# Kernel tuning notes

Measured on AMD Instinct MI355X. Metric: run time of the kernel, lower is better.

## Reference

```python
import jax, jax.numpy as jnp
import numpy as np
from jax import lax

EPS = 1e-5
K = 3  # DCN kernel size


def _conv(x, w, pad, lhs_dil=(1, 1)):
    return lax.conv_general_dilated(
        x, w, window_strides=(1, 1), padding=((pad, pad), (pad, pad)),
        lhs_dilation=lhs_dil, dimension_numbers=('NCHW', 'OIHW', 'NCHW'))


def _batchnorm(x, gamma, beta):
    # training-mode BN (batch statistics), matching nn.BatchNorm2d in train()
    m = jnp.mean(x, axis=(0, 2, 3), keepdims=True)
    v = jnp.var(x, axis=(0, 2, 3), keepdims=True)
    return (x - m) * lax.rsqrt(v + EPS) * gamma[None, :, None, None] + beta[None, :, None, None]


def _bilinear_sample(x, py, px):
    # x: [B,C,H,W]; py,px: [B,K2,H,W] fractional sample coords (zero-pad outside)
    B, C, H, W = x.shape
    K2 = py.shape[1]
    y0 = jnp.floor(py)
    x0 = jnp.floor(px)
    wy = (py - y0)[:, None]  # [B,1,K2,H,W]
    wx = (px - x0)[:, None]
    xf = x.reshape(B, C, H * W)

    def gather(yi, xi):
        valid = ((yi >= 0) & (yi <= H - 1) & (xi >= 0) & (xi <= W - 1)).astype(x.dtype)
        yc = jnp.clip(yi, 0, H - 1).astype(jnp.int32)
        xc = jnp.clip(xi, 0, W - 1).astype(jnp.int32)
        idx = (yc * W + xc).reshape(B, 1, -1)
        v = jnp.take_along_axis(xf, idx, axis=2).reshape(B, C, K2, H, W)
        return v * valid[:, None]

    v00 = gather(y0, x0)
    v01 = gather(y0, x0 + 1)
    v10 = gather(y0 + 1, x0)
    v11 = gather(y0 + 1, x0 + 1)
    return (v00 * (1 - wy) * (1 - wx) + v01 * (1 - wy) * wx
            + v10 * wy * (1 - wx) + v11 * wy * wx)  # [B,C,K2,H,W]


def _dcn(x, w_off, b_off, w_dcn, b_dcn):
    # Modulated deformable conv (DCNv2), stride 1, pad 1, dil 1, 1 deform group
    B, C, H, W = x.shape
    K2 = K * K
    om = _conv(x, w_off, pad=1) + b_off[None, :, None, None]  # [B,3*K2,H,W]
    dy, dx, m = om[:, :K2], om[:, K2:2 * K2], jax.nn.sigmoid(om[:, 2 * K2:])
    ki, kj = jnp.meshgrid(jnp.arange(K), jnp.arange(K), indexing='ij')
    ky = (ki.reshape(-1) - 1).astype(x.dtype)[None, :, None, None]
    kx = (kj.reshape(-1) - 1).astype(x.dtype)[None, :, None, None]
    py = dy + jnp.arange(H, dtype=x.dtype)[None, None, :, None] + ky
    px = dx + jnp.arange(W, dtype=x.dtype)[None, None, None, :] + kx
    val = _bilinear_sample(x, py, px) * m[:, None]  # [B,C,K2,H,W]
    Co = w_dcn.shape[0]
    out = jnp.einsum('bikhw,oik->bohw', val, w_dcn.reshape(Co, C, K2))
    return out + b_dcn[None, :, None, None]


def _conv_transpose(x, w_up):
    # torch ConvTranspose2d(k=4, stride=2, pad=1), weight [Cin, Cout, 4, 4]
    w = jnp.flip(w_up, axis=(2, 3)).transpose(1, 0, 2, 3)  # -> OIHW
    return _conv(x, w, pad=2, lhs_dil=(2, 2))


def setup_inputs() -> dict:
    key = jax.random.key(0)
    ks = jax.random.split(key, 8)
    B, Cin, Cout, H, W = 4, 256, 256, 64, 64
    x = jax.random.normal(ks[0], (B, Cin, H, W), dtype=jnp.float32)
    w_off = jax.random.normal(ks[1], (3 * K * K, Cin, K, K), dtype=jnp.float32) * 0.01
    b_off = jnp.zeros((3 * K * K,), dtype=jnp.float32)
    w_dcn = jax.random.normal(ks[2], (Cout, Cin, K, K), dtype=jnp.float32) * (1.0 / np.sqrt(Cin * K * K))
    b_dcn = jnp.zeros((Cout,), dtype=jnp.float32)
    gamma1 = jax.random.uniform(ks[3], (Cout,), dtype=jnp.float32, minval=0.5, maxval=1.5)
    beta1 = jax.random.normal(ks[4], (Cout,), dtype=jnp.float32) * 0.1
    w_up = jax.random.normal(ks[5], (Cout, Cout, 4, 4), dtype=jnp.float32) * (1.0 / np.sqrt(Cout * 16))
    gamma2 = jax.random.uniform(ks[6], (Cout,), dtype=jnp.float32, minval=0.5, maxval=1.5)
    beta2 = jax.random.normal(ks[7], (Cout,), dtype=jnp.float32) * 0.1
    return {'x': x, 'w_off': w_off, 'b_off': b_off, 'w_dcn': w_dcn, 'b_dcn': b_dcn,
            'gamma1': gamma1, 'beta1': beta1, 'w_up': w_up, 'gamma2': gamma2, 'beta2': beta2}


def reference(x, w_off, b_off, w_dcn, b_dcn, gamma1, beta1, w_up, gamma2, beta2):
    out = _dcn(x, w_off, b_off, w_dcn, b_dcn)
    out = jax.nn.relu(_batchnorm(out, gamma1, beta1))
    out = _conv_transpose(out, w_up)
    out = jax.nn.relu(_batchnorm(out, gamma2, beta2))
    return out
```

## Files before the change

### kernel.cpp

```cpp
#include <hip/hip_runtime.h>
#include <hip/hip_bf16.h>
#include <math.h>

#define B_   4
#define CIN  256
#define COUT 256
#define HW   4096

typedef __attribute__((ext_vector_type(8))) short short8;
typedef __attribute__((ext_vector_type(4))) float float4v;

#define LSTR  40
#define LSTR2 72
#define LSTR4 136

__device__ __forceinline__ float sigmoidf_(float v){ return 1.0f/(1.0f+expf(-v)); }
__device__ __forceinline__ ushort f2bf(float f){
  union { float f; unsigned u; } x; x.f = f;
  unsigned r = x.u + 0x7fffu + ((x.u>>16)&1u);
  return (ushort)(r>>16);
}
__device__ __forceinline__ float bflo(unsigned u){ union{unsigned u; float f;} c; c.u = u<<16;          return c.f; }
__device__ __forceinline__ float bfhi(unsigned u){ union{unsigned u; float f;} c; c.u = u & 0xffff0000u; return c.f; }

__global__ void k_transpose_x(const float* __restrict__ x, ushort* __restrict__ xtb){
  __shared__ float ts[32][33];
  int tx = threadIdx.x & 31, ty = threadIdx.x >> 5;
  int p0 = blockIdx.x * 32, c0 = blockIdx.y * 32, b = blockIdx.z;
  const float* xb = x + (size_t)b*CIN*HW;
#pragma unroll
  for(int q=0;q<4;q++){
    int c = ty + q*8;
    ts[c][tx] = xb[(size_t)(c0+c)*HW + p0+tx];
  }
  __syncthreads();
#pragma unroll
  for(int q=0;q<4;q++){
    int pr = ty + q*8;
    xtb[((size_t)(b*HW + p0+pr)<<8) + c0+tx] = f2bf(ts[tx][pr]);
  }
}

__global__ void k_build_all(const float* __restrict__ w_off, const float* __restrict__ w_dcn,
                            const float* __restrict__ w_up,
                            ushort* __restrict__ Wob, ushort* __restrict__ Wdb,
                            ushort* __restrict__ WT2c){
  int bid = blockIdx.x;
  if(bid < 288){
    int f = bid*256 + threadIdx.x;
    int kc = f>>10, o = (f>>5)&31, kk = f&31;
    int k = kc*32 + kk, tap = k>>8, c = k&255;
    float v = (o < 27) ? w_off[(size_t)o*2304 + c*9 + tap] : 0.f;
    Wob[f] = f2bf(v);
  } else if(bid < 288+2304){
    int f = (bid-288)*256 + threadIdx.x;
    int kc = f>>13, o = (f>>5)&255, kk = f&31;
    int k = kc>>3, c = ((kc&7)<<5) | kk;
    Wdb[f] = f2bf(w_dcn[(size_t)o*2304 + c*9 + k]);
  } else {
    int f = (bid-2592)*256 + threadIdx.x;
    int pp = f>>18, kc = (f>>13)&31, o = (f>>5)&255, kk = f&31;
    int k = kc*32 + kk, ab = k>>8, c = k&255;
    int a = ab>>1, bb = ab&1, ph = pp>>1, pw = pp&1;
    WT2c[f] = f2bf(w_up[(size_t)(c*COUT+o)*16 + (3-ph-2*a)*4 + (3-pw-2*bb)]);
  }
}

__global__ __launch_bounds__(256) void k_offset_mfma(const ushort* __restrict__ xtb,
                        const ushort* __restrict__ Wob, float* __restrict__ om2){
  __shared__ ushort Vs[2][64*LSTR4];
  __shared__ int sIdx[576];
  int tid = threadIdx.x;
  int fb  = blockIdx.x + (blockIdx.y<<6);
  int b   = (fb&7)>>1;
  int px0 = ((((fb>>3)<<1) | (fb&1))) << 6;
  int z   = blockIdx.z;
  for(int t=tid; t<576; t+=256){
    int tap = t>>6, px = t&63;
    int p = px0+px, hh = p>>6, ww = p&63;
    int ih = hh + tap/3 - 1, iw = ww + tap%3 - 1;
    sIdx[t] = (ih>=0 && ih<64 && iw>=0 && iw<64) ? ((b*HW + ih*64+iw)<<8) : -1;
  }
  __syncthreads();

  int lane = tid&63, wv = tid>>6, lo = lane&15, hi = lane>>4;
  float4v acc[2];
  acc[0] = acc[1] = (float4v){0.f,0.f,0.f,0.f};
  int vpx = tid>>2, vseg = tid&3;
  const int wlane = lo*32 + hi*8;

#define OFF_WLOAD_ALLQ(Q, W) do{ \
    _Pragma("unroll") \
    for(int c_=0;c_<4;c_++){ \
      const ushort* wp_ = Wob + (((Q)*4+c_)<<10) + wlane; \
      W[2*c_+0] = *(const short8*)(wp_); \
      W[2*c_+1] = *(const short8*)(wp_ + 512); \
    } \
  }while(0)

#define OFF_GATHER_Q(Q, V) do{ \
    int k_ = (Q)>>1, c0_ = ((Q)&1)<<7; \
    int idx_ = sIdx[(k_<<6)+vpx]; \
    int coff_ = c0_ + (vseg<<5); \
    V[0]=make_uint4(0,0,0,0); V[1]=make_uint4(0,0,0,0); \
    V[2]=make_uint4(0,0,0,0); V[3]=make_uint4(0,0,0,0); \
    if(idx_ >= 0){ \
      V[0] = *(const uint4*)(xtb + idx_ + coff_); \
      V[1] = *(const uint4*)(xtb + idx_ + coff_ + 8); \
      V[2] = *(const uint4*)(xtb + idx_ + coff_ + 16); \
      V[3] = *(const uint4*)(xtb + idx_ + coff_ + 24); \
    } \
  }while(0)

#define OFF_VWRITE_Q(V, BUF) do{ \
    ushort* vp_ = &Vs[BUF][vpx*LSTR4 + (vseg<<5)]; \
    *(uint4*)(vp_)      = V[0]; \
    *(uint4*)(vp_ + 8)  = V[1]; \
    *(uint4*)(vp_ + 16) = V[2]; \
    *(uint4*)(vp_ + 24) = V[3]; \
  }while(0)

#define OFF_COMPUTE_Q2(W, BUF) do{ \
    const ushort* bp_ = &Vs[BUF][(wv*16+lo)*LSTR4 + hi*8]; \
    _Pragma("unroll") \
    for(int c_=0;c_<4;c_++){ \
      short8 ba_ = *(const short8*)(bp_ + c_*32); \
      acc[0] = __builtin_amdgcn_mfma_f32_16x16x32_bf16(W[2*c_+0], ba_, acc[0], 0,0,0); \
      acc[1] = __builtin_amdgcn_mfma_f32_16x16x32_bf16(W[2*c_+1], ba_, acc[1], 0,0,0); \
    } \
  }while(0)

  short8 w[8];
  uint4 vE[4];
  OFF_GATHER_Q(z*9, vE);
  OFF_VWRITE_Q(vE, 0);
  __syncthreads();

#pragma unroll 1
  for(int pc=0; pc<9; ++pc){
    int cur = pc&1;
    int q = z*9 + pc;
    OFF_WLOAD_ALLQ(q, w);
    if(pc<8) OFF_GATHER_Q(q+1, vE);
    OFF_COMPUTE_Q2(w, cur);
    if(pc<8) OFF_VWRITE_Q(vE, cur^1);
    __syncthreads();
  }
  int p = px0 + wv*16 + lo;
#pragma unroll
  for(int mi=0;mi<2;mi++){
    int ob = mi*16 + hi*4;
    float4v a = (mi==0) ? acc[0] : acc[1];
#pragma unroll
    for(int r=0;r<4;r++){
      int o = ob + r;
      if(o < 27) om2[(size_t)((z*B_+b)*27+o)*HW + p] = a[r];
    }
  }
}

#define DCN_WLOAD_ALLQ(Q, W) do{ \
    _Pragma("unroll") \
    for(int c_=0;c_<4;c_++){ \
      const ushort* wp_ = Wdb + ((size_t)((Q)*4+c_)<<13) + wlane; \
      W[4*c_+0] = *(const short8*)(wp_); \
      W[4*c_+1] = *(const short8*)(wp_ + 512); \
      W[4*c_+2] = *(const short8*)(wp_ + 1024); \
      W[4*c_+3] = *(const short8*)(wp_ + 1536); \
    } \
  }while(0)

#define DCN_GATHER_Q(Q, C, CF) do{ \
    int k_ = (Q)>>1, c0_ = ((Q)&1)<<7; \
    int t_ = (k_<<6) + vpx; \
    int pk_ = sPk[t_]; CF = sCf[t_]; \
    int coff_ = c0_ + (vseg<<4); \
    int iy0_=pk_&63, iy1_=(pk_>>6)&63, ix0_=(pk_>>12)&63, ix1_=(pk_>>18)&63; \
    const ushort* p00_ = xtb + cbase + (((iy0_<<6)+ix0_)<<8) + coff_; \
    const ushort* p01_ = xtb + cbase + (((iy0_<<6)+ix1_)<<8) + coff_; \
    const ushort* p10_ = xtb + cbase + (((iy1_<<6)+ix0_)<<8) + coff_; \
    const ushort* p11_ = xtb + cbase + (((iy1_<<6)+ix1_)<<8) + coff_; \
    C[0] = *(const uint4*)(p00_);     C[4] = *(const uint4*)(p00_ + 8); \
    C[1] = *(const uint4*)(p01_);     C[5] = *(const uint4*)(p01_ + 8); \
    C[2] = *(const uint4*)(p10_);     C[6] = *(const uint4*)(p10_ + 8); \
    C[3] = *(const uint4*)(p11_);     C[7] = *(const uint4*)(p11_ + 8); \
  }while(0)

#define DCN_BLEND_H(C0,C1,C2,C3, CF, DST) do{ \
    union{ ushort us[8]; uint4 q; } rr_; \
    rr_.us[0] = f2bf(CF.x*bflo(C0.x)+CF.y*bflo(C1.x)+CF.z*bflo(C2.x)+CF.w*bflo(C3.x)); \
    rr_.us[1] = f2bf(CF.x*bfhi(C0.x)+CF.y*bfhi(C1.x)+CF.z*bfhi(C2.x)+CF.w*bfhi(C3.x)); \
    rr_.us[2] = f2bf(CF.x*bflo(C0.y)+CF.y*bflo(C1.y)+CF.z*bflo(C2.y)+CF.w*bflo(C3.y)); \
    rr_.us[3] = f2bf(CF.x*bfhi(C0.y)+CF.y*bfhi(C1.y)+CF.z*bfhi(C2.y)+CF.w*bfhi(C3.y)); \
    rr_.us[4] = f2bf(CF.x*bflo(C0.z)+CF.y*bflo(C1.z)+CF.z*bflo(C2.z)+CF.w*bflo(C3.z)); \
    rr_.us[5] = f2bf(CF.x*bfhi(C0.z)+CF.y*bfhi(C1.z)+CF.z*bfhi(C2.z)+CF.w*bfhi(C3.z)); \
    rr_.us[6] = f2bf(CF.x*bflo(C0.w)+CF.y*bflo(C1.w)+CF.z*bflo(C2.w)+CF.w*bflo(C3.w)); \
    rr_.us[7] = f2bf(CF.x*bfhi(C0.w)+CF.y*bfhi(C1.w)+CF.z*bfhi(C2.w)+CF.w*bfhi(C3.w)); \
    *(uint4*)(DST) = rr_.q; \
  }while(0)

#define DCN_BLEND_Q(C, CF, BUF) do{ \
    ushort* dp_ = &Vs[BUF][vpx*LSTR4 + (vseg<<4)]; \
    DCN_BLEND_H(C[0],C[1],C[2],C[3], CF, dp_); \
    DCN_BLEND_H(C[4],C[5],C[6],C[7], CF, dp_ + 8); \
  }while(0)

#define DCN_COMPUTE_Q2(W, BUF) do{ \
    const ushort* bp_ = &Vs[BUF][(pn0+lo)*LSTR4 + hi*8]; \
    _Pragma("unroll") \
    for(int c_=0;c_<4;c_++){ \
      short8 b0_ = *(const short8*)(bp_ + c_*32); \
      short8 b1_ = *(const short8*)(bp_ + c_*32 + 16*LSTR4); \
      acc[0][0] = __builtin_amdgcn_mfma_f32_16x16x32_bf16(W[4*c_+0], b0_, acc[0][0], 0,0,0); \
      acc[0][1] = __builtin_amdgcn_mfma_f32_16x16x32_bf16(W[4*c_+0], b1_, acc[0][1], 0,0,0); \
      acc[1][0] = __builtin_amdgcn_mfma_f32_16x16x32_bf16(W[4*c_+1], b0_, acc[1][0], 0,0,0); \
      acc[1][1] = __builtin_amdgcn_mfma_f32_16x16x32_bf16(W[4*c_+1], b1_, acc[1][1], 0,0,0); \
      acc[2][0] = __builtin_amdgcn_mfma_f32_16x16x32_bf16(W[4*c_+2], b0_, acc[2][0], 0,0,0); \
      acc[2][1] = __builtin_amdgcn_mfma_f32_16x16x32_bf16(W[4*c_+2], b1_, acc[2][1], 0,0,0); \
      acc[3][0] = __builtin_amdgcn_mfma_f32_16x16x32_bf16(W[4*c_+3], b0_, acc[3][0], 0,0,0); \
      acc[3][1] = __builtin_amdgcn_mfma_f32_16x16x32_bf16(W[4*c_+3], b1_, acc[3][1], 0,0,0); \
    } \
  }while(0)

__global__ __launch_bounds__(512) void k_dcn_mfma(const ushort* __restrict__ xtb,
                        const float* __restrict__ om2, const float* __restrict__ b_off,
                        const ushort* __restrict__ Wdb, ushort* __restrict__ out1u){
  __shared__ ushort Vs[2][64*LSTR4];
  __shared__ int    sPk[576];
  __shared__ float4 sCf[576];
  int tid = threadIdx.x;
  int fb  = blockIdx.x + (blockIdx.y<<6);
  int b   = (fb&7)>>1;
  int px0 = ((((fb>>3)<<1) | (fb&1))) << 6;
  int z   = blockIdx.z;

  for(int t=tid; t<576; t+=512){
    int k = t>>6, px = t&63;
    int p = px0 + px, hh = p>>6, ww = p&63;
    const float* oma = om2 + (size_t)b*27*HW + p;
    const float* omb = oma + (size_t)B_*27*HW;
    float dy = oma[(size_t)k*HW]      + omb[(size_t)k*HW]      + b_off[k];
    float dx = oma[(size_t)(9+k)*HW]  + omb[(size_t)(9+k)*HW]  + b_off[9+k];
    float mo = sigmoidf_(oma[(size_t)(18+k)*HW] + omb[(size_t)(18+k)*HW] + b_off[18+k]);
    float py  = dy + (float)(hh + k/3 - 1);
    float pxf = dx + (float)(ww + k%3 - 1);
    float y0 = floorf(py), x0 = floorf(pxf);
    float wy = py - y0, wx = pxf - x0;
    float y1 = y0 + 1.0f, x1 = x0 + 1.0f;
    bool vy0 = (y0>=0.f)&&(y0<=63.f), vy1 = (y1>=0.f)&&(y1<=63.f);
    bool vx0 = (x0>=0.f)&&(x0<=63.f), vx1 = (x1>=0.f)&&(x1<=63.f);
    int iy0 = (int)fminf(fmaxf(y0,0.f),63.f);
    int iy1 = (int)fminf(fmaxf(y1,0.f),63.f);
    int ix0 = (int)fminf(fmaxf(x0,0.f),63.f);
    int ix1 = (int)fminf(fmaxf(x1,0.f),63.f);
    sPk[t] = iy0 | (iy1<<6) | (ix0<<12) | (ix1<<18);
    sCf[t] = make_float4((vy0&&vx0)? (1.f-wy)*(1.f-wx)*mo : 0.f,
                         (vy0&&vx1)? (1.f-wy)*wx*mo       : 0.f,
                         (vy1&&vx0)? wy*(1.f-wx)*mo       : 0.f,
                         (vy1&&vx1)? wy*wx*mo             : 0.f);
  }
  __syncthreads();

  int lane = tid&63, wv = tid>>6, lo = lane&15, hi = lane>>4;
  int om0 = (wv>>1)*64, pn0 = (wv&1)*32;
  float4v acc[4][2];
#pragma unroll
  for(int i=0;i<4;i++)
#pragma unroll
    for(int j=0;j<2;j++) acc[i][j] = (float4v){0.f,0.f,0.f,0.f};
  int cbase = (b*HW)<<8;
  int vpx = tid>>3, vseg = tid&7;
  const int wlane = (om0+lo)*32 + hi*8;

  short8 w[16];
  uint4 cE[8];
  float4 fE;

  DCN_GATHER_Q(z*9, cE, fE);
  DCN_BLEND_Q(cE, fE, 0);
  __syncthreads();

#pragma unroll 1
  for(int pc=0; pc<9; ++pc){
    int cur = pc&1;
    int q = z*9 + pc;
    DCN_WLOAD_ALLQ(q, w);
    if(pc<8) DCN_GATHER_Q(q+1, cE, fE);
    DCN_COMPUTE_Q2(w, cur);
    if(pc<8) DCN_BLEND_Q(cE, fE, cur^1);
    __syncthreads();
  }

  ushort* op0 = out1u + ((size_t)((z*B_+b)*COUT)<<12) + px0 + pn0 + lo;
#pragma unroll
  for(int i=0;i<4;i++){
    int ob = om0 + i*16 + hi*4;
#pragma unroll
    for(int r=0;r<4;r++){
      int o = ob + r;
      ushort* op = op0 + ((size_t)o<<12);
#pragma unroll
      for(int j=0;j<2;j++) op[j*16] = f2bf(acc[i][j][r]);
    }
  }
}

__global__ void k_bn_stats_bf2(const ushort* __restrict__ out1u, float* __restrict__ stats){
  int o = blockIdx.x, tid = threadIdx.x;
  float s=0.f, ss=0.f;
  for(int b=0;b<B_;b++){
    const ushort* pa = out1u + ((size_t)(b*COUT+o)<<12);
    const ushort* pb = pa + ((size_t)B_*COUT<<12);
    for(int i=tid*8; i<4096; i+=2048){
      uint4 va = *(const uint4*)(pa + i);
      uint4 vb = *(const uint4*)(pb + i);
      float f;
      f=bflo(va.x)+bflo(vb.x); s+=f; ss+=f*f;  f=bfhi(va.x)+bfhi(vb.x); s+=f; ss+=f*f;
      f=bflo(va.y)+bflo(vb.y); s+=f; ss+=f*f;  f=bfhi(va.y)+bfhi(vb.y); s+=f; ss+=f*f;
      f=bflo(va.z)+bflo(vb.z); s+=f; ss+=f*f;  f=bfhi(va.z)+bfhi(vb.z); s+=f; ss+=f*f;
      f=bflo(va.w)+bflo(vb.w); s+=f; ss+=f*f;  f=bfhi(va.w)+bfhi(vb.w); s+=f; ss+=f*f;
    }
  }
  __shared__ float rs[256], rss[256];
  rs[tid]=s; rss[tid]=ss; __syncthreads();
  for(int st=128; st>0; st>>=1){
    if(tid<st){ rs[tid]+=rs[tid+st]; rss[tid]+=rss[tid+st]; }
    __syncthreads();
  }
  if(tid==0){
    float n = (float)(B_*HW);
    float mean = rs[0]/n;
    float var  = rss[0]/n - mean*mean;
    stats[o*2] = mean; stats[o*2+1] = rsqrtf(var + 1e-5f);
  }
}

__global__ void k_bn_stats_ct(const ushort* __restrict__ ct, float* __restrict__ stats){
  int o = blockIdx.x, tid = threadIdx.x;
  float s=0.f, ss=0.f;
  for(int pl=0; pl<16; ++pl){
    const ushort* p = ct + (((size_t)(pl*256 + o))<<12);
    for(int i=tid*8; i<4096; i+=2048){
      uint4 v = *(const uint4*)(p + i);
      float f;
      f=bflo(v.x); s+=f; ss+=f*f;  f=bfhi(v.x); s+=f; ss+=f*f;
      f=bflo(v.y); s+=f; ss+=f*f;  f=bfhi(v.y); s+=f; ss+=f*f;
      f=bflo(v.z); s+=f; ss+=f*f;  f=bfhi(v.z); s+=f; ss+=f*f;
      f=bflo(v.w); s+=f; ss+=f*f;  f=bfhi(v.w); s+=f; ss+=f*f;
    }
  }
  __shared__ float rs[256], rss[256];
  rs[tid]=s; rss[tid]=ss; __syncthreads();
  for(int st=128; st>0; st>>=1){
    if(tid<st){ rs[tid]+=rs[tid+st]; rss[tid]+=rss[tid+st]; }
    __syncthreads();
  }
  if(tid==0){
    float n = (float)(16*4096);
    float mean = rs[0]/n;
    float var  = rss[0]/n - mean*mean;
    stats[o*2] = mean; stats[o*2+1] = rsqrtf(var + 1e-5f);
  }
}

__global__ void k_bn1_apply_t(const ushort* __restrict__ out1u, const float* __restrict__ stats,
                              const float* __restrict__ gamma, const float* __restrict__ beta,
                              ushort* __restrict__ y1b){
  __shared__ float ts[32][33];
  int tx = threadIdx.x & 31, ty = threadIdx.x >> 5;
  int p0 = blockIdx.x*32, o0 = blockIdx.y*32, b = blockIdx.z;
#pragma unroll
  for(int q=0;q<4;q++){
    int oo = ty + q*8; int o = o0 + oo;
    float m = stats[o*2], rstd = stats[o*2+1];
    float scale = rstd * gamma[o];
    float shift = beta[o] - m * scale;
    size_t idx = ((size_t)(b*COUT+o)<<12) + p0+tx;
    float v = bflo((unsigned)out1u[idx]) + bflo((unsigned)out1u[idx + ((size_t)B_*COUT<<12)]);
    ts[oo][tx] = fmaxf(v*scale + shift, 0.f);
  }
  __syncthreads();
#pragma unroll
  for(int q=0;q<4;q++){
    int pr = ty + q*8;
    y1b[((size_t)(b*HW + p0+pr)<<8) + o0+tx] = f2bf(ts[tx][pr]);
  }
}

__global__ __launch_bounds__(512) void k_convt_mfma(const ushort* __restrict__ y1b,
                        const ushort* __restrict__ WT2c,
                        ushort* __restrict__ ct){
  __shared__ ushort Vs[2][256*LSTR2];
  __shared__ int sIdx[1024];
  int tid = threadIdx.x;
  int fb  = blockIdx.x + (blockIdx.y<<4) + (blockIdx.z<<6);
  int jj = fb&7, rr2 = fb>>3;
  int b   = jj>>1;
  int pp  = ((rr2>>4)<<1) | (jj&1);
  int px0 = (rr2&15) << 8;
  int ph = pp>>1, pw = pp&1;

  for(int t=tid; t<1024; t+=512){
    int ab = t>>8, px = t&255;
    int a = ab>>1, bb = ab&1;
    int p = px0+px, r = p>>6, s = p&63;
    int ih = r + ph - 1 + a, iw = s + pw - 1 + bb;
    sIdx[t] = (ih>=0 && ih<64 && iw>=0 && iw<64) ? ((b*HW + ih*64+iw)<<8) : -1;
  }
  __syncthreads();

  int lane = tid&63, wv = tid>>6, lo = lane&15, hi = lane>>4;
  int om0 = (wv>>1)*64;
  int pn0 = (wv&1)*128;
  float4v acc[4][8];
#pragma unroll
  for(int i=0;i<4;i++)
#pragma unroll
    for(int j=0;j<8;j++) acc[i][j] = (float4v){0.f,0.f,0.f,0.f};

  const ushort* wbase = WT2c + ((size_t)pp<<18);
  const int wlaneb = (om0+lo)*32 + hi*8;
  int vpx = tid>>1, vseg = tid&1;
  uint4 vpre[4];

#define CT3_PREFETCH(PC) do{ \
    int kc0_ = (PC)*2; \
    int ab_ = kc0_>>3, c0_ = (kc0_&7)<<5; \
    int idx_ = sIdx[(ab_<<8) + vpx]; \
    int co_ = c0_ + vseg*32; \
    vpre[0]=make_uint4(0,0,0,0); vpre[1]=make_uint4(0,0,0,0); \
    vpre[2]=make_uint4(0,0,0,0); vpre[3]=make_uint4(0,0,0,0); \
    if(idx_ >= 0){ \
      vpre[0] = *(const uint4*)(y1b + idx_ + co_); \
      vpre[1] = *(const uint4*)(y1b + idx_ + co_ + 8); \
      vpre[2] = *(const uint4*)(y1b + idx_ + co_ + 16); \
      vpre[3] = *(const uint4*)(y1b + idx_ + co_ + 24); \
    } \
  }while(0)

#define CT3_WRITE(BUF) do{ \
    ushort* vp_ = &Vs[BUF][vpx*LSTR2 + vseg*32]; \
    *(uint4*)(vp_)      = vpre[0]; \
    *(uint4*)(vp_ + 8)  = vpre[1]; \
    *(uint4*)(vp_ + 16) = vpre[2]; \
    *(uint4*)(vp_ + 24) = vpre[3]; \
  }while(0)

  CT3_PREFETCH(0);
  CT3_WRITE(0);
  __syncthreads();

#pragma unroll 1
  for(int pc=0; pc<16; ++pc){
    int cur = pc&1;
    if(pc < 15) CT3_PREFETCH(pc+1);
#pragma unroll
    for(int c=0; c<2; ++c){
      const ushort* wp = wbase + ((size_t)(((pc<<1)|c))<<13) + wlaneb;
      const ushort* bp = &Vs[cur][(pn0+lo)*LSTR2 + c*32 + hi*8];
      short8 bfr[8];
#pragma unroll
      for(int j=0;j<8;j++) bfr[j] = *(const short8*)(bp + j*16*LSTR2);
#pragma unroll
      for(int i=0;i<4;i++){
        short8 afr = *(const short8*)(wp + i*512);
#pragma unroll
        for(int j=0;j<8;j++)
          acc[i][j] = __builtin_amdgcn_mfma_f32_16x16x32_bf16(afr, bfr[j], acc[i][j], 0,0,0);
      }
    }
    if(pc < 15) CT3_WRITE(cur^1);
    __syncthreads();
  }

  ushort* cb = ct + (((size_t)(pp*4 + b)*256)<<12);
#pragma unroll
  for(int i=0;i<4;i++){
#pragma unroll
    for(int r=0;r<4;r++){
      int o = om0 + i*16 + hi*4 + r;
      ushort* row = cb + ((size_t)o<<12) + px0 + pn0 + lo;
#pragma unroll
      for(int j=0;j<8;j++) row[j*16] = f2bf(acc[i][j][r]);
    }
  }
}

__global__ void k_bn2_apply(const ushort* __restrict__ ct, const float* __restrict__ stats,
                            const float* __restrict__ gamma, const float* __restrict__ beta,
                            float* __restrict__ out){
  int gid = blockIdx.x*256 + threadIdx.x;
  int e4 = gid<<2;
  int b = e4>>22, o = (e4>>14)&255, q = e4&16383;
  int H2 = q>>7, W2 = q&127;
  int r = H2>>1, ph = H2&1, s0 = W2>>1;
  size_t base0 = (((size_t)((ph*2)*4 + b)*256 + o)<<12) + r*64 + s0;
  unsigned u0 = *(const unsigned*)(ct + base0);
  unsigned u1 = *(const unsigned*)(ct + base0 + ((size_t)4<<20));
  float m = stats[o*2], rstd = stats[o*2+1];
  float sc = rstd * gamma[o];
  float sh = beta[o] - m * sc;
  float4 v;
  v.x = fmaxf(bflo(u0)*sc + sh, 0.f);
  v.y = fmaxf(bflo(u1)*sc + sh, 0.f);
  v.z = fmaxf(bfhi(u0)*sc + sh, 0.f);
  v.w = fmaxf(bfhi(u1)*sc + sh, 0.f);
  *(float4*)(out + e4) = v;
}

extern "C" void kernel_launch(void* const* d_in, const int* in_sizes, int n_in,
                              void* d_out, int out_size, void* d_ws, size_t ws_size,
                              hipStream_t stream){
  (void)in_sizes; (void)n_in; (void)out_size; (void)ws_size;
  const float* x     = (const float*)d_in[0];
  const float* w_off = (const float*)d_in[1];
  const float* b_off = (const float*)d_in[2];
  const float* w_dcn = (const float*)d_in[3];
  const float* gamma1= (const float*)d_in[5];
  const float* beta1 = (const float*)d_in[6];
  const float* w_up  = (const float*)d_in[7];
  const float* gamma2= (const float*)d_in[8];
  const float* beta2 = (const float*)d_in[9];
  float* out = (float*)d_out;

  float* ws    = (float*)d_ws;
  ushort* ct   = (ushort*)ws;
  float* om2   = ws;
  ushort* xtb  = (ushort*)(ws + 884736);
  ushort* out1u= (ushort*)(ws + 884736 + 2097152);
  float* base2 = ws + 8388608;
  ushort* y1b  = (ushort*)base2;
  ushort* WT2c = (ushort*)(base2 + 2097152);
  ushort* Wdb  = (ushort*)(base2 + 2097152 + 524288);
  ushort* Wob  = (ushort*)(base2 + 2097152 + 524288 + 294912);
  float* st1   = base2 + 2097152 + 524288 + 294912 + 36864;
  float* st2   = st1 + 512;

  k_transpose_x <<<dim3(128,8,4), 256, 0, stream>>>(x, xtb);
  k_build_all   <<<6688, 256, 0, stream>>>(w_off, w_dcn, w_up, Wob, Wdb, WT2c);
  k_offset_mfma <<<dim3(64,4,2), 256, 0, stream>>>(xtb, Wob, om2);
  k_dcn_mfma    <<<dim3(64,4,2), 512, 0, stream>>>(xtb, om2, b_off, Wdb, out1u);
  k_bn_stats_bf2<<<256,  256, 0, stream>>>(out1u, st1);
  k_bn1_apply_t <<<dim3(128,8,4), 256, 0, stream>>>(out1u, st1, gamma1, beta1, y1b);
  k_convt_mfma  <<<dim3(16,4,4),  512, 0, stream>>>(y1b, WT2c, ct);
  k_bn_stats_ct <<<256,  256, 0, stream>>>(ct, st2);
  k_bn2_apply   <<<16384,256, 0, stream>>>(ct, st2, gamma2, beta2, out);
}
```

Measured before the change: 257.6 us.

## Fuse BN statistics into GEMM epilogues and drop DCN split-K

Batch-norm sum and sum-of-squares are now accumulated with wave shuffles and atomics in the epilogues of the DCN and transposed-conv kernels, so the two separate stats kernels and their re-reads of the outputs go away. The DCN kernel no longer splits K across two z-slices; each block runs all 18 chunks and writes a single output, so bn1_apply reads only one buffer. The trade-off is half as many DCN blocks (less parallelism), float atomic contention, and variance computed from raw sums in fp32.

```diff
diff --git a/kernel.cpp b/kernel.cpp
--- a/kernel.cpp
+++ b/kernel.cpp
@@ -44,8 +44,14 @@
 __global__ void k_build_all(const float* __restrict__ w_off, const float* __restrict__ w_dcn,
                             const float* __restrict__ w_up,
                             ushort* __restrict__ Wob, ushort* __restrict__ Wdb,
-                            ushort* __restrict__ WT2c){
+                            ushort* __restrict__ WT2c,
+                            float* __restrict__ st1raw, float* __restrict__ st2raw){
   int bid = blockIdx.x;
+  if(bid == 0 && threadIdx.x < 256){
+    int t = threadIdx.x;
+    st1raw[t] = 0.f; st1raw[256+t] = 0.f;
+    st2raw[t] = 0.f; st2raw[256+t] = 0.f;
+  }
   if(bid < 288){
     int f = bid*256 + threadIdx.x;
     int kc = f>>10, o = (f>>5)&31, kk = f&31;
@@ -224,7 +230,8 @@
 
 __global__ __launch_bounds__(512) void k_dcn_mfma(const ushort* __restrict__ xtb,
                         const float* __restrict__ om2, const float* __restrict__ b_off,
-                        const ushort* __restrict__ Wdb, ushort* __restrict__ out1u){
+                        const ushort* __restrict__ Wdb, ushort* __restrict__ out1u,
+                        float* __restrict__ st1raw){
   __shared__ ushort Vs[2][64*LSTR4];
   __shared__ int    sPk[576];
   __shared__ float4 sCf[576];
@@ -232,7 +239,6 @@
   int fb  = blockIdx.x + (blockIdx.y<<6);
   int b   = (fb&7)>>1;
   int px0 = ((((fb>>3)<<1) | (fb&1))) << 6;
-  int z   = blockIdx.z;
 
   for(int t=tid; t<576; t+=512){
     int k = t>>6, px = t&63;
@@ -276,22 +282,21 @@
   uint4 cE[8];
   float4 fE;
 
-  DCN_GATHER_Q(z*9, cE, fE);
+  DCN_GATHER_Q(0, cE, fE);
   DCN_BLEND_Q(cE, fE, 0);
   __syncthreads();
 
 #pragma unroll 1
-  for(int pc=0; pc<9; ++pc){
+  for(int pc=0; pc<18; ++pc){
     int cur = pc&1;
-    int q = z*9 + pc;
-    DCN_WLOAD_ALLQ(q, w);
-    if(pc<8) DCN_GATHER_Q(q+1, cE, fE);
+    DCN_WLOAD_ALLQ(pc, w);
+    if(pc<17) DCN_GATHER_Q(pc+1, cE, fE);
     DCN_COMPUTE_Q2(w, cur);
-    if(pc<8) DCN_BLEND_Q(cE, fE, cur^1);
+    if(pc<17) DCN_BLEND_Q(cE, fE, cur^1);
     __syncthreads();
   }
 
-  ushort* op0 = out1u + ((size_t)((z*B_+b)*COUT)<<12) + px0 + pn0 + lo;
+  ushort* op0 = out1u + ((size_t)(b*COUT)<<12) + px0 + pn0 + lo;
 #pragma unroll
   for(int i=0;i<4;i++){
     int ob = om0 + i*16 + hi*4;
@@ -299,84 +304,37 @@
     for(int r=0;r<4;r++){
       int o = ob + r;
       ushort* op = op0 + ((size_t)o<<12);
-#pragma unroll
-      for(int j=0;j<2;j++) op[j*16] = f2bf(acc[i][j][r]);
+      float v0 = acc[i][0][r], v1 = acc[i][1][r];
+      op[0]  = f2bf(v0);
+      op[16] = f2bf(v1);
+      float s  = v0 + v1;
+      float q2 = v0*v0 + v1*v1;
+#pragma unroll
+      for(int st=1; st<16; st<<=1){ s += __shfl_xor(s, st); q2 += __shfl_xor(q2, st); }
+      if(lo == 0){
+        atomicAdd(&st1raw[2*o],   s);
+        atomicAdd(&st1raw[2*o+1], q2);
+      }
     }
   }
 }
 
-__global__ void k_bn_stats_bf2(const ushort* __restrict__ out1u, float* __restrict__ stats){
-  int o = blockIdx.x, tid = threadIdx.x;
-  float s=0.f, ss=0.f;
-  for(int b=0;b<B_;b++){
-    const ushort* pa = out1u + ((size_t)(b*COUT+o)<<12);
-    const ushort* pb = pa + ((size_t)B_*COUT<<12);
-    for(int i=tid*8; i<4096; i+=2048){
-      uint4 va = *(const uint4*)(pa + i);
-      uint4 vb = *(const uint4*)(pb + i);
-      float f;
-      f=bflo(va.x)+bflo(vb.x); s+=f; ss+=f*f;  f=bfhi(va.x)+bfhi(vb.x); s+=f; ss+=f*f;
-      f=bflo(va.y)+bflo(vb.y); s+=f; ss+=f*f;  f=bfhi(va.y)+bfhi(vb.y); s+=f; ss+=f*f;
-      f=bflo(va.z)+bflo(vb.z); s+=f; ss+=f*f;  f=bfhi(va.z)+bfhi(vb.z); s+=f; ss+=f*f;
-      f=bflo(va.w)+bflo(vb.w); s+=f; ss+=f*f;  f=bfhi(va.w)+bfhi(vb.w); s+=f; ss+=f*f;
-    }
-  }
-  __shared__ float rs[256], rss[256];
-  rs[tid]=s; rss[tid]=ss; __syncthreads();
-  for(int st=128; st>0; st>>=1){
-    if(tid<st){ rs[tid]+=rs[tid+st]; rss[tid]+=rss[tid+st]; }
-    __syncthreads();
-  }
-  if(tid==0){
-    float n = (float)(B_*HW);
-    float mean = rs[0]/n;
-    float var  = rss[0]/n - mean*mean;
-    stats[o*2] = mean; stats[o*2+1] = rsqrtf(var + 1e-5f);
-  }
-}
-
-__global__ void k_bn_stats_ct(const ushort* __restrict__ ct, float* __restrict__ stats){
-  int o = blockIdx.x, tid = threadIdx.x;
-  float s=0.f, ss=0.f;
-  for(int pl=0; pl<16; ++pl){
-    const ushort* p = ct + (((size_t)(pl*256 + o))<<12);
-    for(int i=tid*8; i<4096; i+=2048){
-      uint4 v = *(const uint4*)(p + i);
-      float f;
-      f=bflo(v.x); s+=f; ss+=f*f;  f=bfhi(v.x); s+=f; ss+=f*f;
-      f=bflo(v.y); s+=f; ss+=f*f;  f=bfhi(v.y); s+=f; ss+=f*f;
-      f=bflo(v.z); s+=f; ss+=f*f;  f=bfhi(v.z); s+=f; ss+=f*f;
-      f=bflo(v.w); s+=f; ss+=f*f;  f=bfhi(v.w); s+=f; ss+=f*f;
-    }
-  }
-  __shared__ float rs[256], rss[256];
-  rs[tid]=s; rss[tid]=ss; __syncthreads();
-  for(int st=128; st>0; st>>=1){
-    if(tid<st){ rs[tid]+=rs[tid+st]; rss[tid]+=rss[tid+st]; }
-    __syncthreads();
-  }
-  if(tid==0){
-    float n = (float)(16*4096);
-    float mean = rs[0]/n;
-    float var  = rss[0]/n - mean*mean;
-    stats[o*2] = mean; stats[o*2+1] = rsqrtf(var + 1e-5f);
-  }
-}
-
-__global__ void k_bn1_apply_t(const ushort* __restrict__ out1u, const float* __restrict__ stats,
+__global__ void k_bn1_apply_t(const ushort* __restrict__ out1u, const float* __restrict__ st1raw,
                               const float* __restrict__ gamma, const float* __restrict__ beta,
                               ushort* __restrict__ y1b){
   __shared__ float ts[32][33];
   int tx = threadIdx.x & 31, ty = threadIdx.x >> 5;
   int p0 = blockIdx.x*32, o0 = blockIdx.y*32, b = blockIdx.z;
+  const float inv_n = 1.f/16384.f;
 #pragma unroll
   for(int q=0;q<4;q++){
     int oo = ty + q*8; int o = o0 + oo;
-    float m = stats[o*2], rstd = stats[o*2+1];
+    float mean = st1raw[2*o] * inv_n;
+    float var  = st1raw[2*o+1] * inv_n - mean*mean;
+    float rstd = rsqrtf(var + 1e-5f);
     float scale = rstd * gamma[o];
-    float shift = beta[o] - m * scale;
-    size_t idx = ((size_t)(b*COUT+o)<<12) + p0+tx;
-    float v = bflo((unsigned)out1u[idx]) + bflo((unsigned)out1u[idx + ((size_t)B_*COUT<<12)]);
+    float shift = beta[o] - mean * scale;
+    float v = bflo((unsigned)out1u[((size_t)(b*COUT+o)<<12) + p0+tx]);
     ts[oo][tx] = fmaxf(v*scale + shift, 0.f);
   }
   __syncthreads();
@@ -389,7 +347,7 @@
 
 __global__ __launch_bounds__(512) void k_convt_mfma(const ushort* __restrict__ y1b,
                         const ushort* __restrict__ WT2c,
-                        ushort* __restrict__ ct){
+                        ushort* __restrict__ ct, float* __restrict__ st2raw){
   __shared__ ushort Vs[2][256*LSTR2];
   __shared__ int sIdx[1024];
   int tid = threadIdx.x;
@@ -480,13 +438,24 @@
     for(int r=0;r<4;r++){
       int o = om0 + i*16 + hi*4 + r;
       ushort* row = cb + ((size_t)o<<12) + px0 + pn0 + lo;
-#pragma unroll
-      for(int j=0;j<8;j++) row[j*16] = f2bf(acc[i][j][r]);
+      float s = 0.f, q2 = 0.f;
+#pragma unroll
+      for(int j=0;j<8;j++){
+        float v = acc[i][j][r];
+        row[j*16] = f2bf(v);
+        s += v; q2 += v*v;
+      }
+#pragma unroll
+      for(int st=1; st<16; st<<=1){ s += __shfl_xor(s, st); q2 += __shfl_xor(q2, st); }
+      if(lo == 0){
+        atomicAdd(&st2raw[2*o],   s);
+        atomicAdd(&st2raw[2*o+1], q2);
+      }
     }
   }
 }
 
-__global__ void k_bn2_apply(const ushort* __restrict__ ct, const float* __restrict__ stats,
+__global__ void k_bn2_apply(const ushort* __restrict__ ct, const float* __restrict__ st2raw,
                             const float* __restrict__ gamma, const float* __restrict__ beta,
                             float* __restrict__ out){
   int gid = blockIdx.x*256 + threadIdx.x;
@@ -497,9 +466,11 @@
   size_t base0 = (((size_t)((ph*2)*4 + b)*256 + o)<<12) + r*64 + s0;
   unsigned u0 = *(const unsigned*)(ct + base0);
   unsigned u1 = *(const unsigned*)(ct + base0 + ((size_t)4<<20));
-  float m = stats[o*2], rstd = stats[o*2+1];
+  const float inv_n = 1.f/65536.f;
+  float mean = st2raw[2*o] * inv_n;
+  float rstd = rsqrtf(st2raw[2*o+1]*inv_n - mean*mean + 1e-5f);
   float sc = rstd * gamma[o];
-  float sh = beta[o] - m * sc;
+  float sh = beta[o] - mean * sc;
   float4 v;
   v.x = fmaxf(bflo(u0)*sc + sh, 0.f);
   v.y = fmaxf(bflo(u1)*sc + sh, 0.f);
@@ -533,16 +504,14 @@
   ushort* WT2c = (ushort*)(base2 + 2097152);
   ushort* Wdb  = (ushort*)(base2 + 2097152 + 524288);
   ushort* Wob  = (ushort*)(base2 + 2097152 + 524288 + 294912);
-  float* st1   = base2 + 2097152 + 524288 + 294912 + 36864;
-  float* st2   = st1 + 512;
+  float* st1raw= base2 + 2097152 + 524288 + 294912 + 36864;
+  float* st2raw= st1raw + 512;
 
   k_transpose_x <<<dim3(128,8,4), 256, 0, stream>>>(x, xtb);
-  k_build_all   <<<6688, 256, 0, stream>>>(w_off, w_dcn, w_up, Wob, Wdb, WT2c);
+  k_build_all   <<<6688, 256, 0, stream>>>(w_off, w_dcn, w_up, Wob, Wdb, WT2c, st1raw, st2raw);
   k_offset_mfma <<<dim3(64,4,2), 256, 0, stream>>>(xtb, Wob, om2);
-  k_dcn_mfma    <<<dim3(64,4,2), 512, 0, stream>>>(xtb, om2, b_off, Wdb, out1u);
-  k_bn_stats_bf2<<<256,  256, 0, stream>>>(out1u, st1);
-  k_bn1_apply_t <<<dim3(128,8,4), 256, 0, stream>>>(out1u, st1, gamma1, beta1, y1b);
-  k_convt_mfma  <<<dim3(16,4,4),  512, 0, stream>>>(y1b, WT2c, ct);
-  k_bn_stats_ct <<<256,  256, 0, stream>>>(ct, st2);
-  k_bn2_apply   <<<16384,256, 0, stream>>>(ct, st2, gamma2, beta2, out);
-}
+  k_dcn_mfma    <<<dim3(64,4),   512, 0, stream>>>(xtb, om2, b_off, Wdb, out1u, st1raw);
+  k_bn1_apply_t <<<dim3(128,8,4), 256, 0, stream>>>(out1u, st1raw, gamma1, beta1, y1b);
+  k_convt_mfma  <<<dim3(16,4,4),  512, 0, stream>>>(y1b, WT2c, ct, st2raw);
+  k_bn2_apply   <<<16384,256, 0, stream>>>(ct, st2raw, gamma2, beta2, out);
+}
```

Result: slower. 519.1 us (+101.5%).

## Drop split-K in deformable conv; accumulate all 18 chunks per block

Applied to the files above, without the earlier changes.

The DCN MFMA kernel no longer splits the reduction over two z-slices that wrote separate bf16 partial outputs. Each block now loops over all 18 chunks and writes a single output, so the BN stats and BN apply kernels read one buffer instead of summing two. This removes the extra partial-output write and read traffic and one bf16 rounding step. In exchange the grid is halved to 256 blocks, which reduces parallelism and latency hiding on the GPU.

```diff
diff --git a/kernel.cpp b/kernel.cpp
--- a/kernel.cpp
+++ b/kernel.cpp
@@ -232,7 +232,6 @@
   int fb  = blockIdx.x + (blockIdx.y<<6);
   int b   = (fb&7)>>1;
   int px0 = ((((fb>>3)<<1) | (fb&1))) << 6;
-  int z   = blockIdx.z;
 
   for(int t=tid; t<576; t+=512){
     int k = t>>6, px = t&63;
@@ -276,22 +275,21 @@
   uint4 cE[8];
   float4 fE;
 
-  DCN_GATHER_Q(z*9, cE, fE);
+  DCN_GATHER_Q(0, cE, fE);
   DCN_BLEND_Q(cE, fE, 0);
   __syncthreads();
 
 #pragma unroll 1
-  for(int pc=0; pc<9; ++pc){
+  for(int pc=0; pc<18; ++pc){
     int cur = pc&1;
-    int q = z*9 + pc;
-    DCN_WLOAD_ALLQ(q, w);
-    if(pc<8) DCN_GATHER_Q(q+1, cE, fE);
+    DCN_WLOAD_ALLQ(pc, w);
+    if(pc<17) DCN_GATHER_Q(pc+1, cE, fE);
     DCN_COMPUTE_Q2(w, cur);
-    if(pc<8) DCN_BLEND_Q(cE, fE, cur^1);
+    if(pc<17) DCN_BLEND_Q(cE, fE, cur^1);
     __syncthreads();
   }
 
-  ushort* op0 = out1u + ((size_t)((z*B_+b)*COUT)<<12) + px0 + pn0 + lo;
+  ushort* op0 = out1u + ((size_t)(b*COUT)<<12) + px0 + pn0 + lo;
 #pragma unroll
   for(int i=0;i<4;i++){
     int ob = om0 + i*16 + hi*4;
@@ -299,26 +297,24 @@
     for(int r=0;r<4;r++){
       int o = ob + r;
       ushort* op = op0 + ((size_t)o<<12);
-#pragma unroll
-      for(int j=0;j<2;j++) op[j*16] = f2bf(acc[i][j][r]);
+      op[0]  = f2bf(acc[i][0][r]);
+      op[16] = f2bf(acc[i][1][r]);
     }
   }
 }
 
-__global__ void k_bn_stats_bf2(const ushort* __restrict__ out1u, float* __restrict__ stats){
+__global__ void k_bn_stats_bf1(const ushort* __restrict__ out1u, float* __restrict__ stats){
   int o = blockIdx.x, tid = threadIdx.x;
   float s=0.f, ss=0.f;
   for(int b=0;b<B_;b++){
-    const ushort* pa = out1u + ((size_t)(b*COUT+o)<<12);
-    const ushort* pb = pa + ((size_t)B_*COUT<<12);
+    const ushort* p = out1u + ((size_t)(b*COUT+o)<<12);
     for(int i=tid*8; i<4096; i+=2048){
-      uint4 va = *(const uint4*)(pa + i);
-      uint4 vb = *(const uint4*)(pb + i);
+      uint4 v = *(const uint4*)(p + i);
       float f;
-      f=bflo(va.x)+bflo(vb.x); s+=f; ss+=f*f;  f=bfhi(va.x)+bfhi(vb.x); s+=f; ss+=f*f;
-      f=bflo(va.y)+bflo(vb.y); s+=f; ss+=f*f;  f=bfhi(va.y)+bfhi(vb.y); s+=f; ss+=f*f;
-      f=bflo(va.z)+bflo(vb.z); s+=f; ss+=f*f;  f=bfhi(va.z)+bfhi(vb.z); s+=f; ss+=f*f;
-      f=bflo(va.w)+bflo(vb.w); s+=f; ss+=f*f;  f=bfhi(va.w)+bfhi(vb.w); s+=f; ss+=f*f;
+      f=bflo(v.x); s+=f; ss+=f*f;  f=bfhi(v.x); s+=f; ss+=f*f;
+      f=bflo(v.y); s+=f; ss+=f*f;  f=bfhi(v.y); s+=f; ss+=f*f;
+      f=bflo(v.z); s+=f; ss+=f*f;  f=bfhi(v.z); s+=f; ss+=f*f;
+      f=bflo(v.w); s+=f; ss+=f*f;  f=bfhi(v.w); s+=f; ss+=f*f;
     }
   }
   __shared__ float rs[256], rss[256];
@@ -375,8 +371,7 @@
     float m = stats[o*2], rstd = stats[o*2+1];
     float scale = rstd * gamma[o];
     float shift = beta[o] - m * scale;
-    size_t idx = ((size_t)(b*COUT+o)<<12) + p0+tx;
-    float v = bflo((unsigned)out1u[idx]) + bflo((unsigned)out1u[idx + ((size_t)B_*COUT<<12)]);
+    float v = bflo((unsigned)out1u[((size_t)(b*COUT+o)<<12) + p0+tx]);
     ts[oo][tx] = fmaxf(v*scale + shift, 0.f);
   }
   __syncthreads();
@@ -539,8 +534,8 @@
   k_transpose_x <<<dim3(128,8,4), 256, 0, stream>>>(x, xtb);
   k_build_all   <<<6688, 256, 0, stream>>>(w_off, w_dcn, w_up, Wob, Wdb, WT2c);
   k_offset_mfma <<<dim3(64,4,2), 256, 0, stream>>>(xtb, Wob, om2);
-  k_dcn_mfma    <<<dim3(64,4,2), 512, 0, stream>>>(xtb, om2, b_off, Wdb, out1u);
-  k_bn_stats_bf2<<<256,  256, 0, stream>>>(out1u, st1);
+  k_dcn_mfma    <<<dim3(64,4),   512, 0, stream>>>(xtb, om2, b_off, Wdb, out1u);
+  k_bn_stats_bf1<<<256,  256, 0, stream>>>(out1u, st1);
   k_bn1_apply_t <<<dim3(128,8,4), 256, 0, stream>>>(out1u, st1, gamma1, beta1, y1b);
   k_convt_mfma  <<<dim3(16,4,4),  512, 0, stream>>>(y1b, WT2c, ct);
   k_bn_stats_ct <<<256,  256, 0, stream>>>(ct, st2);
```

After: 254.6 us. Within noise of the previous version (-1.2%).
